# Optimization experiments

Hardware: AMD Instinct MI355X
Metric: run time of the kernel (lower is better)

## Reference

```python
import jax, jax.numpy as jnp
import numpy as np


def setup_inputs() -> dict:
    key = jax.random.key(0)
    k1, k2, k3, k4, k5 = jax.random.split(key, 5)
    B, C, H, W = 16, 256, 32, 32
    G = 4
    gd = C // G
    x = jax.random.normal(k1, (B, C, H, W), dtype=jnp.float32)
    # grouped 1x1 convs == per-group [gd, gd] linear maps (torch weight (C, C//G, 1, 1))
    s = 1.0 / np.sqrt(gd)
    wq = jax.random.normal(k2, (G, gd, gd), dtype=jnp.float32) * s
    wk = jax.random.normal(k3, (G, gd, gd), dtype=jnp.float32) * s
    wv = jax.random.normal(k4, (G, gd, gd), dtype=jnp.float32) * s
    wo = jax.random.normal(k5, (C, C), dtype=jnp.float32) * (1.0 / np.sqrt(C))
    return {"x": x, "wq": wq, "wk": wk, "wv": wv, "wo": wo}


def reference(x, wq, wk, wv, wo):
    B, C, H, W = x.shape
    G, gd = wq.shape[0], wq.shape[1]
    N = H * W
    xg = x.reshape(B, G, gd, N)  # split channels into groups, flatten spatial
    # grouped 1x1 conv projections: out[d] = sum_c w[d,c] * x[c] per group
    Q = jnp.einsum('bgcn,gdc->bgdn', xg, wq)
    K = jnp.einsum('bgcn,gdc->bgdn', xg, wk)
    V = jnp.einsum('bgcn,gdc->bgdn', xg, wv)
    scale = 1.0 / (float(gd) ** 0.5)
    # scores: Q^T K over channel dim -> [B, G, N, N]
    scores = jnp.einsum('bgdn,bgdm->bgnm', Q, K) * scale
    attn = jax.nn.softmax(scores, axis=-1)
    # out[d, n] = sum_m attn[n, m] * V[d, m]  (== (attn @ V^T)^T in torch code)
    out = jnp.einsum('bgnm,bgdm->bgdn', attn, V)
    out = out.reshape(B, C, H, W)
    # out_proj: dense 1x1 conv over all channels
    return jnp.einsum('bchw,dc->bdhw', out, wo)
```

## Files before the change

### kernel.cpp

```cpp
#include <hip/hip_runtime.h>
#include <hip/hip_bf16.h>


typedef __bf16 bf16x8 __attribute__((ext_vector_type(8)));
typedef short s16x8 __attribute__((ext_vector_type(8)));
typedef short s16x4 __attribute__((ext_vector_type(4)));
typedef float f32x4 __attribute__((ext_vector_type(4)));

__device__ __forceinline__ unsigned short f2b(float f) {
  unsigned int u = __builtin_bit_cast(unsigned int, f);
  u += 0x7fffu + ((u >> 16) & 1u);
  return (unsigned short)(u >> 16);
}
__device__ __forceinline__ unsigned short bf16u(float f) {
  return __builtin_bit_cast(unsigned short, __float2bfloat16(f));
}
__device__ __forceinline__ f32x4 mfma16(s16x8 a, s16x8 b, f32x4 c) {
  return __builtin_amdgcn_mfma_f32_16x16x32_bf16(
      __builtin_bit_cast(bf16x8, a), __builtin_bit_cast(bf16x8, b), c, 0, 0, 0);
}
__device__ __forceinline__ f32x4 mfma16k16(s16x4 a, s16x4 b, f32x4 c) {
  return __builtin_amdgcn_mfma_f32_16x16x16bf16_1k(a, b, c, 0, 0, 0);
}
__device__ __forceinline__ void gload16(const void* g, void* l) {
  __builtin_amdgcn_global_load_lds((const __attribute__((address_space(1))) void*)g,
                                   (__attribute__((address_space(3))) void*)l, 16, 0, 0);
}
__device__ __forceinline__ void stage8k(const unsigned short* g, short* l, int wid, int lane) {
  gload16(g + wid * 1024 + lane * 8,       l + wid * 1024);
  gload16(g + wid * 1024 + 512 + lane * 8, l + wid * 1024 + 512);
}

__global__ __launch_bounds__(256) void cvt_prep_kernel(
    const float* __restrict__ x, const float* __restrict__ wq, const float* __restrict__ wk,
    const float* __restrict__ wv, const float* __restrict__ wo,
    unsigned short* __restrict__ XbT, unsigned short* __restrict__ Xbs,
    unsigned short* __restrict__ Mts, unsigned short* __restrict__ Ub) {
  __shared__ __align__(16) short T[64][72];
  const int f = blockIdx.x;
  const int tid = threadIdx.x;
  if (f >= 1024) {
    int pb = f - 1024;
    if (pb < 64) {
      int id = pb * 256 + tid;
      int g = id >> 12, e = (id >> 6) & 63, c = id & 63;
      const float* q = wq + g * 4096;
      const float* k = wk + g * 4096;
      float acc = 0.f;
      for (int d = 0; d < 64; ++d) acc += q[d * 64 + c] * k[d * 64 + e];
      Mts[g * 4096 + e * 64 + (c ^ ((e & 7) << 3))] = f2b(acc * 0.125f * 1.4426950408889634f);
    } else {
      int i = (pb - 64) * 256 + tid;
      int o = i >> 8, gc = i & 255, g = gc >> 6, c = gc & 63;
      const float* v = wv + g * 4096;
      const float* w = wo + o * 256 + g * 64;
      float acc = 0.f;
      for (int d = 0; d < 64; ++d) acc += w[d] * v[d * 64 + c];
      Ub[i] = f2b(acc);
    }
    return;
  }
  const int xcd = f & 7;
  const int idx = f >> 3;
  const int head = ((idx & 7) << 3) | xcd;
  const int tile = idx >> 3;
  const int chunk = head * 16 + tile;
  const float* Xg = x + (size_t)head * 65536 + tile * 64;
  for (int i = 0; i < 4; ++i) {
    int row = i * 16 + (tid >> 4);
    int col = (tid & 15) * 4;
    float4 v = *(const float4*)(Xg + (size_t)row * 1024 + col);
    ushort4 s4 = make_ushort4(f2b(v.x), f2b(v.y), f2b(v.z), f2b(v.w));
    *(ushort4*)&T[row][col] = s4;
  }
  __syncthreads();
  unsigned short* oT = XbT + (size_t)chunk * 4096;
  unsigned short* oC = Xbs + (size_t)chunk * 4096;
  for (int p = 0; p < 2; ++p) {
    int idx2 = p * 256 + tid;
    int rr = idx2 >> 3, j = idx2 & 7;
    int sb = (j ^ (rr & 7)) * 8;
    unsigned short w[8];
    for (int i = 0; i < 8; ++i) w[i] = (unsigned short)T[sb + i][rr];
    *(s16x8*)(oT + rr * 64 + j * 8) = *(s16x8*)w;
    s16x8 rv = *(const s16x8*)&T[rr][sb];
    *(s16x8*)(oC + rr * 64 + j * 8) = rv;
  }
}

__global__ __launch_bounds__(256, 2)
void attn_kernel(const unsigned short* __restrict__ XbT, const unsigned short* __restrict__ Xbs,
                 const unsigned short* __restrict__ Mts, unsigned short* __restrict__ Ast) {
  __shared__ __align__(16) short XB[6][4096];

  const int f = blockIdx.x;
  const int bg = (f & 7) + ((f >> 6) << 3);
  const int n0 = ((f >> 3) & 7) * 128;
  const int tid = threadIdx.x;
  const int wid = tid >> 6;
  const int lane = tid & 63;
  const int l15 = lane & 15, l4 = lane >> 4;
  const int swz = (l15 & 7) << 3;
  const int l4h = l4 >> 1, l4l = (l4 & 1) * 4;
  const int nh = wid & 1;
  const int mh = wid >> 1;
  const unsigned short* xtg = XbT + (size_t)bg * 65536;
  const unsigned short* xcg = Xbs + (size_t)bg * 65536;

  stage8k(Mts + (bg & 3) * 4096, &XB[3][0], wid, lane);
  stage8k(xtg + (size_t)(n0 >> 6) * 4096, &XB[0][0], wid, lane);
  stage8k(xtg + (size_t)((n0 >> 6) + 1) * 4096, &XB[1][0], wid, lane);
  __syncthreads();

  s16x8 qpB[4][2];
  {
    s16x8 bm[4][2];
    for (int eb = 0; eb < 4; ++eb)
      for (int kc = 0; kc < 2; ++kc)
        bm[eb][kc] = *(const s16x8*)&XB[3][(eb * 16 + l15) * 64 + ((kc * 32 + l4 * 8) ^ swz)];
    for (int nt = 0; nt < 2; ++nt) {
      int q = wid * 32 + nt * 16;
      int h = q >> 6, rl = (q & 63) + l15;
      int rsw = ((rl & 7) << 3);
      s16x8 a0 = *(const s16x8*)&XB[h][rl * 64 + ((l4 * 8) ^ rsw)];
      s16x8 a1 = *(const s16x8*)&XB[h][rl * 64 + ((32 + l4 * 8) ^ rsw)];
      short* Qs = (q >= 64) ? &XB[5][0] : &XB[2][0];
      for (int eb = 0; eb < 4; ++eb) {
        f32x4 acc0 = {0.f, 0.f, 0.f, 0.f};
        acc0 = mfma16(a0, bm[eb][0], acc0);
        acc0 = mfma16(a1, bm[eb][1], acc0);
        for (int r = 0; r < 4; ++r) {
          int qrow = q + 4 * l4 + r;
          int cb2 = eb * 2 + (l15 >> 3);
          Qs[(qrow & 63) * 64 + (((cb2 ^ (qrow & 7)) << 3) | (l15 & 7))] = (short)bf16u(acc0[r]);
        }
      }
    }
  }
  asm volatile("s_waitcnt lgkmcnt(0)" ::: "memory");
  __builtin_amdgcn_sched_barrier(0);
  __syncthreads();
  {
    const short* Qs = nh ? &XB[5][0] : &XB[2][0];
#pragma unroll
    for (int nt = 0; nt < 4; ++nt) {
      int row = nt * 16 + l15;
#pragma unroll
      for (int kc = 0; kc < 2; ++kc)
        qpB[nt][kc] = *(const s16x8*)&Qs[row * 64 + (((kc * 4 + l4) ^ (l15 & 7)) << 3)];
    }
  }
  __syncthreads();

  stage8k(xtg,        &XB[0][0], wid, lane);
  stage8k(xcg,        &XB[3][0], wid, lane);
  stage8k(xtg + 4096, &XB[1][0], wid, lane);
  stage8k(xcg + 4096, &XB[4][0], wid, lane);

  float rowSp[4];
#pragma unroll
  for (int nt = 0; nt < 4; ++nt) rowSp[nt] = 0.f;
  f32x4 acc[4][4];
#pragma unroll
  for (int nt = 0; nt < 4; ++nt)
#pragma unroll
    for (int cb = 0; cb < 4; ++cb) acc[nt][cb] = (f32x4){0.f, 0.f, 0.f, 0.f};

#define STEP(K, VMC)                                                                    \
  {                                                                                     \
    asm volatile("s_waitcnt vmcnt(" VMC ")" ::: "memory");                              \
    __builtin_amdgcn_s_barrier();                                                       \
    __builtin_amdgcn_sched_barrier(0);                                                  \
    if ((K) < 14) {                                                                     \
      stage8k(xtg + (size_t)((K) + 2) * 4096, &XB[((K) + 2) % 3][0], wid, lane);        \
      stage8k(xcg + (size_t)((K) + 2) * 4096, &XB[3 + ((K) + 2) % 3][0], wid, lane);    \
    }                                                                                   \
    const int cs = (K) % 3;                                                             \
    _Pragma("unroll")                                                                   \
    for (int mb = 0; mb < 2; ++mb) {                                                    \
      const int rmr = (mh * 32 + mb * 16 + l15) * 64;                                   \
      s16x8 xt0 = *(const s16x8*)&XB[cs][rmr + ((l4 * 8) ^ swz)];                       \
      s16x8 xt1 = *(const s16x8*)&XB[cs][rmr + ((32 + l4 * 8) ^ swz)];                  \
      s16x4 ax4[4];                                                                     \
      _Pragma("unroll")                                                                 \
      for (int cb = 0; cb < 4; ++cb) {                                                  \
        int rc = cb * 16 + l15;                                                         \
        ax4[cb] = *(const s16x4*)&XB[3 + cs][rc * 64 +                                  \
                      (((mh * 4 + mb * 2 + l4h) ^ (rc & 7)) << 3) + l4l];               \
      }                                                                                 \
      _Pragma("unroll")                                                                 \
      for (int nt = 0; nt < 4; ++nt) {                                                  \
        f32x4 sv = {0.f, 0.f, 0.f, 0.f};                                                \
        sv = mfma16(xt0, qpB[nt][0], sv);                                               \
        sv = mfma16(xt1, qpB[nt][1], sv);                                               \
        float p0 = __builtin_amdgcn_exp2f(sv[0]);                                       \
        float p1 = __builtin_amdgcn_exp2f(sv[1]);                                       \
        float p2 = __builtin_amdgcn_exp2f(sv[2]);                                       \
        float p3 = __builtin_amdgcn_exp2f(sv[3]);                                       \
        rowSp[nt] += (p0 + p1) + (p2 + p3);                                             \
        unsigned int lo = (unsigned int)bf16u(p0) | ((unsigned int)bf16u(p1) << 16);    \
        unsigned int hi = (unsigned int)bf16u(p2) | ((unsigned int)bf16u(p3) << 16);    \
        uint2 pu; pu.x = lo; pu.y = hi;                                                 \
        s16x4 pb = __builtin_bit_cast(s16x4, pu);                                       \
        _Pragma("unroll")                                                               \
        for (int cb = 0; cb < 4; ++cb)                                                  \
          acc[nt][cb] = mfma16k16(ax4[cb], pb, acc[nt][cb]);                            \
      }                                                                                 \
    }                                                                                   \
  }

  STEP(0, "4")  STEP(1, "4")  STEP(2, "4")  STEP(3, "4")
  STEP(4, "4")  STEP(5, "4")  STEP(6, "4")  STEP(7, "4")
  STEP(8, "4")  STEP(9, "4")  STEP(10, "4") STEP(11, "4")
  STEP(12, "4") STEP(13, "4") STEP(14, "4") STEP(15, "0")
#undef STEP

  __syncthreads();
  float* Scr = (float*)&XB[0][0];

  float rs[4];
#pragma unroll
  for (int nt = 0; nt < 4; ++nt) {
    float t = rowSp[nt];
    t += __shfl_xor(t, 16, 64);
    t += __shfl_xor(t, 32, 64);
    rs[nt] = t;
  }

  if (mh == 1) {
#pragma unroll
    for (int nt = 0; nt < 4; ++nt) {
#pragma unroll
      for (int cb = 0; cb < 4; ++cb) {
        int base = ((nh * 4 + nt) * 4 + cb) * 256;
#pragma unroll
        for (int r = 0; r < 4; ++r)
          Scr[base + (l4 * 4 + r) * 16 + l15] = acc[nt][cb][r];
      }
      if (l4 == 0) Scr[8192 + (nh * 4 + nt) * 16 + l15] = rs[nt];
    }
  }
  __syncthreads();
  if (mh == 0) {
    const int b = bg >> 2, g = bg & 3;
#pragma unroll
    for (int nt = 0; nt < 4; ++nt) {
      float inv = 1.f / (rs[nt] + Scr[8192 + (nh * 4 + nt) * 16 + l15]);
      int n = n0 + nh * 64 + nt * 16 + l15;
      unsigned short* Ag = Ast + ((size_t)(b * 1024 + n)) * 256 + g * 64;
#pragma unroll
      for (int cb = 0; cb < 4; ++cb) {
        int base = ((nh * 4 + nt) * 4 + cb) * 256;
        float v0 = acc[nt][cb][0] + Scr[base + (l4 * 4 + 0) * 16 + l15];
        float v1 = acc[nt][cb][1] + Scr[base + (l4 * 4 + 1) * 16 + l15];
        float v2 = acc[nt][cb][2] + Scr[base + (l4 * 4 + 2) * 16 + l15];
        float v3 = acc[nt][cb][3] + Scr[base + (l4 * 4 + 3) * 16 + l15];
        ushort4 pk = make_ushort4(bf16u(v0 * inv), bf16u(v1 * inv),
                                  bf16u(v2 * inv), bf16u(v3 * inv));
        *(ushort4*)(Ag + cb * 16 + l4 * 4) = pk;
      }
    }
  }
}

__global__ __launch_bounds__(256, 2)
void proj_kernel(const unsigned short* __restrict__ Ub, const unsigned short* __restrict__ Ast,
                 float* __restrict__ out) {
  const int b = blockIdx.z;
  const int o0 = blockIdx.y * 128;
  const int n0 = blockIdx.x * 128;
  const int tid = threadIdx.x;
  const int wid = tid >> 6;
  const int lane = tid & 63;
  const int l15 = lane & 15, l4 = lane >> 4;
  const int ow = o0 + (wid & 1) * 64;
  const int nw = n0 + (wid >> 1) * 64;
  const unsigned short* A_ = Ast + ((size_t)b * 1024 + nw) * 256;

  f32x4 acc[4][4];
  for (int i = 0; i < 4; ++i)
    for (int j = 0; j < 4; ++j) acc[i][j] = (f32x4){0.f, 0.f, 0.f, 0.f};

  for (int kc = 0; kc < 8; ++kc) {
    s16x8 af[4], bfr[4];
    for (int ob = 0; ob < 4; ++ob)
      af[ob] = *(const s16x8*)(Ub + (size_t)(ow + ob * 16 + l15) * 256 + kc * 32 + l4 * 8);
    for (int nb = 0; nb < 4; ++nb)
      bfr[nb] = *(const s16x8*)(A_ + (size_t)(nb * 16 + l15) * 256 + kc * 32 + l4 * 8);
    for (int ob = 0; ob < 4; ++ob)
      for (int nb = 0; nb < 4; ++nb)
        acc[ob][nb] = mfma16(af[ob], bfr[nb], acc[ob][nb]);
  }
  float* O = out + ((size_t)b * 256 + ow) * 1024 + nw;
  for (int ob = 0; ob < 4; ++ob)
    for (int r = 0; r < 4; ++r)
      for (int nb = 0; nb < 4; ++nb)
        O[(size_t)(ob * 16 + l4 * 4 + r) * 1024 + nb * 16 + l15] = acc[ob][nb][r];
}

extern "C" void kernel_launch(void* const* d_in, const int* in_sizes, int n_in,
                              void* d_out, int out_size, void* d_ws, size_t ws_size,
                              hipStream_t stream) {
  const float* x  = (const float*)d_in[0];
  const float* wq = (const float*)d_in[1];
  const float* wk = (const float*)d_in[2];
  const float* wv = (const float*)d_in[3];
  const float* wo = (const float*)d_in[4];
  float* out = (float*)d_out;
  char* ws = (char*)d_ws;
  unsigned short* XbT = (unsigned short*)(ws);
  unsigned short* Xbs = (unsigned short*)(ws + 8388608);
  unsigned short* Mts = (unsigned short*)(ws + 16777216);
  unsigned short* Ub  = (unsigned short*)(ws + 16777216 + 32768);
  unsigned short* Ast = (unsigned short*)(ws + 16777216 + 163840);

  cvt_prep_kernel<<<1344, 256, 0, stream>>>(x, wq, wk, wv, wo, XbT, Xbs, Mts, Ub);
  attn_kernel<<<512, 256, 0, stream>>>(XbT, Xbs, Mts, Ast);
  proj_kernel<<<dim3(8, 2, 16), 256, 0, stream>>>(Ub, Ast, out);
}
```

Measured before the change: 51.68 us.

## Use per-wave private LDS slots with interleaved X layout, drop block barriers in attention loop

Prep now writes X into a combined per-half layout, so each key chunk's transposed and channel-major halves sit next to each other. Each wave in the attention kernel then streams only the half it needs into its own double-buffered LDS slots. This removes the block-wide barrier per step and lets waves run independently. The cost is wave-private loads that duplicate some traffic, plus an lgkmcnt wait before restaging. The projection kernel also halves its N tile per block to launch twice as many blocks.

```diff
diff --git a/kernel.cpp b/kernel.cpp
--- a/kernel.cpp
+++ b/kernel.cpp
@@ -34,8 +34,8 @@
 __global__ __launch_bounds__(256) void cvt_prep_kernel(
     const float* __restrict__ x, const float* __restrict__ wq, const float* __restrict__ wk,
     const float* __restrict__ wv, const float* __restrict__ wo,
-    unsigned short* __restrict__ XbT, unsigned short* __restrict__ Xbs,
-    unsigned short* __restrict__ Mts, unsigned short* __restrict__ Ub) {
+    unsigned short* __restrict__ XbH, unsigned short* __restrict__ Mts,
+    unsigned short* __restrict__ Ub) {
   __shared__ __align__(16) short T[64][72];
   const int f = blockIdx.x;
   const int tid = threadIdx.x;
@@ -64,34 +64,39 @@
   const int idx = f >> 3;
   const int head = ((idx & 7) << 3) | xcd;
   const int tile = idx >> 3;
-  const int chunk = head * 16 + tile;
   const float* Xg = x + (size_t)head * 65536 + tile * 64;
   for (int i = 0; i < 4; ++i) {
-    int row = i * 16 + (tid >> 4);
-    int col = (tid & 15) * 4;
-    float4 v = *(const float4*)(Xg + (size_t)row * 1024 + col);
+    int c = i * 16 + (tid >> 4);
+    int ml = (tid & 15) * 4;
+    float4 v = *(const float4*)(Xg + (size_t)c * 1024 + ml);
     ushort4 s4 = make_ushort4(f2b(v.x), f2b(v.y), f2b(v.z), f2b(v.w));
-    *(ushort4*)&T[row][col] = s4;
-  }
-  __syncthreads();
-  unsigned short* oT = XbT + (size_t)chunk * 4096;
-  unsigned short* oC = Xbs + (size_t)chunk * 4096;
-  for (int p = 0; p < 2; ++p) {
-    int idx2 = p * 256 + tid;
-    int rr = idx2 >> 3, j = idx2 & 7;
-    int sb = (j ^ (rr & 7)) * 8;
-    unsigned short w[8];
-    for (int i = 0; i < 8; ++i) w[i] = (unsigned short)T[sb + i][rr];
-    *(s16x8*)(oT + rr * 64 + j * 8) = *(s16x8*)w;
-    s16x8 rv = *(const s16x8*)&T[rr][sb];
-    *(s16x8*)(oC + rr * 64 + j * 8) = rv;
+    *(ushort4*)&T[c][ml] = s4;
+  }
+  __syncthreads();
+  unsigned short* out = XbH + ((size_t)head * 16 + tile) * 8192;
+  const int half = tid >> 7, rem = tid & 127;
+  {
+    int lr = rem >> 2, cp = (rem & 3) * 2;
+    for (int u = 0; u < 2; ++u) {
+      int cb8 = cp + u, pos = cb8 ^ (lr & 7);
+      unsigned short w[8];
+      for (int ci = 0; ci < 8; ++ci) w[ci] = (unsigned short)T[cb8 * 8 + ci][half * 32 + lr];
+      *(s16x8*)(out + half * 4096 + lr * 64 + pos * 8) = *(s16x8*)w;
+    }
+  }
+  {
+    int c = rem >> 1, j = (rem & 1) * 2;
+    s16x8 v0 = *(const s16x8*)&T[c][half * 32 + j * 8];
+    s16x8 v1 = *(const s16x8*)&T[c][half * 32 + j * 8 + 8];
+    *(s16x8*)(out + half * 4096 + 2048 + c * 32 + ((j ^ (c & 3)) * 8)) = v0;
+    *(s16x8*)(out + half * 4096 + 2048 + c * 32 + (((j + 1) ^ (c & 3)) * 8)) = v1;
   }
 }
 
 __global__ __launch_bounds__(256, 2)
-void attn_kernel(const unsigned short* __restrict__ XbT, const unsigned short* __restrict__ Xbs,
-                 const unsigned short* __restrict__ Mts, unsigned short* __restrict__ Ast) {
-  __shared__ __align__(16) short XB[6][4096];
+void attn_kernel(const unsigned short* __restrict__ XbH, const unsigned short* __restrict__ Mts,
+                 unsigned short* __restrict__ Ast) {
+  __shared__ __align__(16) short L[32768];
 
   const int f = blockIdx.x;
   const int bg = (f & 7) + ((f >> 6) << 3);
@@ -104,12 +109,14 @@
   const int l4h = l4 >> 1, l4l = (l4 & 1) * 4;
   const int nh = wid & 1;
   const int mh = wid >> 1;
-  const unsigned short* xtg = XbT + (size_t)bg * 65536;
-  const unsigned short* xcg = Xbs + (size_t)bg * 65536;
-
-  stage8k(Mts + (bg & 3) * 4096, &XB[3][0], wid, lane);
-  stage8k(xtg + (size_t)(n0 >> 6) * 4096, &XB[0][0], wid, lane);
-  stage8k(xtg + (size_t)((n0 >> 6) + 1) * 4096, &XB[1][0], wid, lane);
+  const unsigned short* xgh = XbH + (size_t)bg * 131072;
+
+  const int c0 = n0 >> 6;
+  stage8k(Mts + (bg & 3) * 4096, &L[0], wid, lane);
+  stage8k(xgh + (size_t)c0 * 8192,            &L[4096],  wid, lane);
+  stage8k(xgh + (size_t)c0 * 8192 + 4096,     &L[8192],  wid, lane);
+  stage8k(xgh + (size_t)(c0 + 1) * 8192,      &L[12288], wid, lane);
+  stage8k(xgh + (size_t)(c0 + 1) * 8192 + 4096, &L[16384], wid, lane);
   __syncthreads();
 
   s16x8 qpB[4][2];
@@ -117,22 +124,22 @@
     s16x8 bm[4][2];
     for (int eb = 0; eb < 4; ++eb)
       for (int kc = 0; kc < 2; ++kc)
-        bm[eb][kc] = *(const s16x8*)&XB[3][(eb * 16 + l15) * 64 + ((kc * 32 + l4 * 8) ^ swz)];
-    for (int nt = 0; nt < 2; ++nt) {
-      int q = wid * 32 + nt * 16;
-      int h = q >> 6, rl = (q & 63) + l15;
-      int rsw = ((rl & 7) << 3);
-      s16x8 a0 = *(const s16x8*)&XB[h][rl * 64 + ((l4 * 8) ^ rsw)];
-      s16x8 a1 = *(const s16x8*)&XB[h][rl * 64 + ((32 + l4 * 8) ^ rsw)];
-      short* Qs = (q >= 64) ? &XB[5][0] : &XB[2][0];
+        bm[eb][kc] = *(const s16x8*)&L[(eb * 16 + l15) * 64 + ((kc * 32 + l4 * 8) ^ swz)];
+    for (int nt2 = 0; nt2 < 2; ++nt2) {
+      int q0 = wid * 32 + nt2 * 16;
+      int base = 4096 + (q0 >> 6) * 8192 + ((q0 >> 5) & 1) * 4096;
+      int rl = (q0 & 31) + l15;
+      s16x8 a0 = *(const s16x8*)&L[base + rl * 64 + ((l4 * 8) ^ swz)];
+      s16x8 a1 = *(const s16x8*)&L[base + rl * 64 + ((32 + l4 * 8) ^ swz)];
+      short* Qs = &L[20480 + (q0 >= 64 ? 4096 : 0)];
       for (int eb = 0; eb < 4; ++eb) {
-        f32x4 acc0 = {0.f, 0.f, 0.f, 0.f};
-        acc0 = mfma16(a0, bm[eb][0], acc0);
-        acc0 = mfma16(a1, bm[eb][1], acc0);
+        f32x4 a = {0.f, 0.f, 0.f, 0.f};
+        a = mfma16(a0, bm[eb][0], a);
+        a = mfma16(a1, bm[eb][1], a);
         for (int r = 0; r < 4; ++r) {
-          int qrow = q + 4 * l4 + r;
+          int qrow = q0 + 4 * l4 + r;
           int cb2 = eb * 2 + (l15 >> 3);
-          Qs[(qrow & 63) * 64 + (((cb2 ^ (qrow & 7)) << 3) | (l15 & 7))] = (short)bf16u(acc0[r]);
+          Qs[(qrow & 63) * 64 + (((cb2 ^ (qrow & 7)) << 3) | (l15 & 7))] = (short)bf16u(a[r]);
         }
       }
     }
@@ -141,7 +148,7 @@
   __builtin_amdgcn_sched_barrier(0);
   __syncthreads();
   {
-    const short* Qs = nh ? &XB[5][0] : &XB[2][0];
+    const short* Qs = &L[20480 + (nh ? 4096 : 0)];
 #pragma unroll
     for (int nt = 0; nt < 4; ++nt) {
       int row = nt * 16 + l15;
@@ -152,10 +159,19 @@
   }
   __syncthreads();
 
-  stage8k(xtg,        &XB[0][0], wid, lane);
-  stage8k(xcg,        &XB[3][0], wid, lane);
-  stage8k(xtg + 4096, &XB[1][0], wid, lane);
-  stage8k(xcg + 4096, &XB[4][0], wid, lane);
+  const unsigned short* xgw = xgh + mh * 4096;
+  short* slot0 = &L[wid * 8192];
+  short* slot1 = &L[wid * 8192 + 4096];
+
+#define STAGEP(K, SL)                                                                   \
+  {                                                                                     \
+    const unsigned short* g_ = xgw + (size_t)(K) * 8192;                                \
+    _Pragma("unroll")                                                                   \
+    for (int i = 0; i < 8; ++i) gload16(g_ + i * 512 + lane * 8, (SL) + i * 512);       \
+  }
+
+  STAGEP(0, slot0)
+  STAGEP(1, slot1)
 
   float rowSp[4];
 #pragma unroll
@@ -169,24 +185,19 @@
 #define STEP(K, VMC)                                                                    \
   {                                                                                     \
     asm volatile("s_waitcnt vmcnt(" VMC ")" ::: "memory");                              \
-    __builtin_amdgcn_s_barrier();                                                       \
     __builtin_amdgcn_sched_barrier(0);                                                  \
-    if ((K) < 14) {                                                                     \
-      stage8k(xtg + (size_t)((K) + 2) * 4096, &XB[((K) + 2) % 3][0], wid, lane);        \
-      stage8k(xcg + (size_t)((K) + 2) * 4096, &XB[3 + ((K) + 2) % 3][0], wid, lane);    \
-    }                                                                                   \
-    const int cs = (K) % 3;                                                             \
+    short* cs = ((K) & 1) ? slot1 : slot0;                                              \
     _Pragma("unroll")                                                                   \
     for (int mb = 0; mb < 2; ++mb) {                                                    \
-      const int rmr = (mh * 32 + mb * 16 + l15) * 64;                                   \
-      s16x8 xt0 = *(const s16x8*)&XB[cs][rmr + ((l4 * 8) ^ swz)];                       \
-      s16x8 xt1 = *(const s16x8*)&XB[cs][rmr + ((32 + l4 * 8) ^ swz)];                  \
+      int rml = mb * 16 + l15;                                                          \
+      s16x8 xt0 = *(const s16x8*)&cs[rml * 64 + ((l4 * 8) ^ swz)];                      \
+      s16x8 xt1 = *(const s16x8*)&cs[rml * 64 + ((32 + l4 * 8) ^ swz)];                 \
       s16x4 ax4[4];                                                                     \
       _Pragma("unroll")                                                                 \
       for (int cb = 0; cb < 4; ++cb) {                                                  \
         int rc = cb * 16 + l15;                                                         \
-        ax4[cb] = *(const s16x4*)&XB[3 + cs][rc * 64 +                                  \
-                      (((mh * 4 + mb * 2 + l4h) ^ (rc & 7)) << 3) + l4l];               \
+        ax4[cb] = *(const s16x4*)&cs[2048 + rc * 32 +                                   \
+                        (((mb * 2 + l4h) ^ (rc & 3)) << 3) + l4l];                      \
       }                                                                                 \
       _Pragma("unroll")                                                                 \
       for (int nt = 0; nt < 4; ++nt) {                                                  \
@@ -207,16 +218,21 @@
           acc[nt][cb] = mfma16k16(ax4[cb], pb, acc[nt][cb]);                            \
       }                                                                                 \
     }                                                                                   \
-  }
-
-  STEP(0, "4")  STEP(1, "4")  STEP(2, "4")  STEP(3, "4")
-  STEP(4, "4")  STEP(5, "4")  STEP(6, "4")  STEP(7, "4")
-  STEP(8, "4")  STEP(9, "4")  STEP(10, "4") STEP(11, "4")
-  STEP(12, "4") STEP(13, "4") STEP(14, "4") STEP(15, "0")
+    if ((K) <= 13) {                                                                    \
+      asm volatile("s_waitcnt lgkmcnt(0)" ::: "memory");                                \
+      STAGEP((K) + 2, cs)                                                               \
+    }                                                                                   \
+  }
+
+  STEP(0, "8")  STEP(1, "8")  STEP(2, "8")  STEP(3, "8")
+  STEP(4, "8")  STEP(5, "8")  STEP(6, "8")  STEP(7, "8")
+  STEP(8, "8")  STEP(9, "8")  STEP(10, "8") STEP(11, "8")
+  STEP(12, "8") STEP(13, "8") STEP(14, "8") STEP(15, "0")
 #undef STEP
-
-  __syncthreads();
-  float* Scr = (float*)&XB[0][0];
+#undef STAGEP
+
+  __syncthreads();
+  float* Scr = (float*)&L[0];
 
   float rs[4];
 #pragma unroll
@@ -268,33 +284,33 @@
                  float* __restrict__ out) {
   const int b = blockIdx.z;
   const int o0 = blockIdx.y * 128;
-  const int n0 = blockIdx.x * 128;
+  const int n0 = blockIdx.x * 64;
   const int tid = threadIdx.x;
   const int wid = tid >> 6;
   const int lane = tid & 63;
   const int l15 = lane & 15, l4 = lane >> 4;
   const int ow = o0 + (wid & 1) * 64;
-  const int nw = n0 + (wid >> 1) * 64;
+  const int nw = n0 + (wid >> 1) * 32;
   const unsigned short* A_ = Ast + ((size_t)b * 1024 + nw) * 256;
 
-  f32x4 acc[4][4];
+  f32x4 acc[4][2];
   for (int i = 0; i < 4; ++i)
-    for (int j = 0; j < 4; ++j) acc[i][j] = (f32x4){0.f, 0.f, 0.f, 0.f};
+    for (int j = 0; j < 2; ++j) acc[i][j] = (f32x4){0.f, 0.f, 0.f, 0.f};
 
   for (int kc = 0; kc < 8; ++kc) {
-    s16x8 af[4], bfr[4];
+    s16x8 af[4], bfr[2];
     for (int ob = 0; ob < 4; ++ob)
       af[ob] = *(const s16x8*)(Ub + (size_t)(ow + ob * 16 + l15) * 256 + kc * 32 + l4 * 8);
-    for (int nb = 0; nb < 4; ++nb)
+    for (int nb = 0; nb < 2; ++nb)
       bfr[nb] = *(const s16x8*)(A_ + (size_t)(nb * 16 + l15) * 256 + kc * 32 + l4 * 8);
     for (int ob = 0; ob < 4; ++ob)
-      for (int nb = 0; nb < 4; ++nb)
+      for (int nb = 0; nb < 2; ++nb)
         acc[ob][nb] = mfma16(af[ob], bfr[nb], acc[ob][nb]);
   }
   float* O = out + ((size_t)b * 256 + ow) * 1024 + nw;
   for (int ob = 0; ob < 4; ++ob)
     for (int r = 0; r < 4; ++r)
-      for (int nb = 0; nb < 4; ++nb)
+      for (int nb = 0; nb < 2; ++nb)
         O[(size_t)(ob * 16 + l4 * 4 + r) * 1024 + nb * 16 + l15] = acc[ob][nb][r];
 }
 
@@ -308,13 +324,12 @@
   const float* wo = (const float*)d_in[4];
   float* out = (float*)d_out;
   char* ws = (char*)d_ws;
-  unsigned short* XbT = (unsigned short*)(ws);
-  unsigned short* Xbs = (unsigned short*)(ws + 8388608);
+  unsigned short* XbH = (unsigned short*)(ws);
   unsigned short* Mts = (unsigned short*)(ws + 16777216);
   unsigned short* Ub  = (unsigned short*)(ws + 16777216 + 32768);
   unsigned short* Ast = (unsigned short*)(ws + 16777216 + 163840);
 
-  cvt_prep_kernel<<<1344, 256, 0, stream>>>(x, wq, wk, wv, wo, XbT, Xbs, Mts, Ub);
-  attn_kernel<<<512, 256, 0, stream>>>(XbT, Xbs, Mts, Ast);
-  proj_kernel<<<dim3(8, 2, 16), 256, 0, stream>>>(Ub, Ast, out);
-}
+  cvt_prep_kernel<<<1344, 256, 0, stream>>>(x, wq, wk, wv, wo, XbH, Mts, Ub);
+  attn_kernel<<<512, 256, 0, stream>>>(XbH, Mts, Ast);
+  proj_kernel<<<dim3(16, 2, 16), 256, 0, stream>>>(Ub, Ast, out);
+}
```

New measurement: 58.00 us. +12.2%, slower.

## Halve attention query tile to 64, double-buffer LDS, and split key range across warps

Applied to the files above, without the earlier changes.

The attention kernel now processes 64 query rows per block instead of 128, doubling the grid to 1024 blocks. LDS shrinks from six to four 8K buffers with double buffering instead of triple, and launch bounds rise to 3 blocks per CU. All four warps share the queries and each takes a quarter of the keys, so the cross-warp reduction becomes a three-way sum done in two phases through LDS. The projection kernel's n-tile is also halved, doubling its grid. The aim is more occupancy and parallelism, at the cost of shallower prefetch, redundant K/V loading per block and extra reduction syncs.

```diff
diff --git a/kernel.cpp b/kernel.cpp
--- a/kernel.cpp
+++ b/kernel.cpp
@@ -88,60 +88,58 @@
   }
 }
 
-__global__ __launch_bounds__(256, 2)
+__global__ __launch_bounds__(256, 3)
 void attn_kernel(const unsigned short* __restrict__ XbT, const unsigned short* __restrict__ Xbs,
                  const unsigned short* __restrict__ Mts, unsigned short* __restrict__ Ast) {
-  __shared__ __align__(16) short XB[6][4096];
+  __shared__ __align__(16) short L[16384];
 
   const int f = blockIdx.x;
-  const int bg = (f & 7) + ((f >> 6) << 3);
-  const int n0 = ((f >> 3) & 7) * 128;
+  const int xcd = f & 7;
+  const int qt = (f >> 3) & 15;
+  const int bg = xcd + ((f >> 7) << 3);
+  const int n0 = qt * 64;
   const int tid = threadIdx.x;
   const int wid = tid >> 6;
   const int lane = tid & 63;
   const int l15 = lane & 15, l4 = lane >> 4;
   const int swz = (l15 & 7) << 3;
   const int l4h = l4 >> 1, l4l = (l4 & 1) * 4;
-  const int nh = wid & 1;
-  const int mh = wid >> 1;
+  const int rm = wid * 16 + l15;
   const unsigned short* xtg = XbT + (size_t)bg * 65536;
   const unsigned short* xcg = Xbs + (size_t)bg * 65536;
 
-  stage8k(Mts + (bg & 3) * 4096, &XB[3][0], wid, lane);
-  stage8k(xtg + (size_t)(n0 >> 6) * 4096, &XB[0][0], wid, lane);
-  stage8k(xtg + (size_t)((n0 >> 6) + 1) * 4096, &XB[1][0], wid, lane);
+  stage8k(Mts + (bg & 3) * 4096, &L[0], wid, lane);
+  stage8k(xtg + (size_t)qt * 4096, &L[4096], wid, lane);
   __syncthreads();
 
   s16x8 qpB[4][2];
   {
     s16x8 bm[4][2];
+#pragma unroll
     for (int eb = 0; eb < 4; ++eb)
+#pragma unroll
       for (int kc = 0; kc < 2; ++kc)
-        bm[eb][kc] = *(const s16x8*)&XB[3][(eb * 16 + l15) * 64 + ((kc * 32 + l4 * 8) ^ swz)];
-    for (int nt = 0; nt < 2; ++nt) {
-      int q = wid * 32 + nt * 16;
-      int h = q >> 6, rl = (q & 63) + l15;
-      int rsw = ((rl & 7) << 3);
-      s16x8 a0 = *(const s16x8*)&XB[h][rl * 64 + ((l4 * 8) ^ rsw)];
-      s16x8 a1 = *(const s16x8*)&XB[h][rl * 64 + ((32 + l4 * 8) ^ rsw)];
-      short* Qs = (q >= 64) ? &XB[5][0] : &XB[2][0];
-      for (int eb = 0; eb < 4; ++eb) {
-        f32x4 acc0 = {0.f, 0.f, 0.f, 0.f};
-        acc0 = mfma16(a0, bm[eb][0], acc0);
-        acc0 = mfma16(a1, bm[eb][1], acc0);
-        for (int r = 0; r < 4; ++r) {
-          int qrow = q + 4 * l4 + r;
-          int cb2 = eb * 2 + (l15 >> 3);
-          Qs[(qrow & 63) * 64 + (((cb2 ^ (qrow & 7)) << 3) | (l15 & 7))] = (short)bf16u(acc0[r]);
-        }
+        bm[eb][kc] = *(const s16x8*)&L[(eb * 16 + l15) * 64 + ((kc * 32 + l4 * 8) ^ swz)];
+    int rl = wid * 16 + l15;
+    s16x8 a0 = *(const s16x8*)&L[4096 + rl * 64 + ((l4 * 8) ^ swz)];
+    s16x8 a1 = *(const s16x8*)&L[4096 + rl * 64 + ((32 + l4 * 8) ^ swz)];
+    short* Qs = &L[8192];
+#pragma unroll
+    for (int eb = 0; eb < 4; ++eb) {
+      f32x4 a = {0.f, 0.f, 0.f, 0.f};
+      a = mfma16(a0, bm[eb][0], a);
+      a = mfma16(a1, bm[eb][1], a);
+#pragma unroll
+      for (int r = 0; r < 4; ++r) {
+        int qrow = wid * 16 + 4 * l4 + r;
+        int cb2 = eb * 2 + (l15 >> 3);
+        Qs[qrow * 64 + (((cb2 ^ (qrow & 7)) << 3) | (l15 & 7))] = (short)bf16u(a[r]);
       }
     }
   }
-  asm volatile("s_waitcnt lgkmcnt(0)" ::: "memory");
-  __builtin_amdgcn_sched_barrier(0);
   __syncthreads();
   {
-    const short* Qs = nh ? &XB[5][0] : &XB[2][0];
+    const short* Qs = &L[8192];
 #pragma unroll
     for (int nt = 0; nt < 4; ++nt) {
       int row = nt * 16 + l15;
@@ -152,10 +150,8 @@
   }
   __syncthreads();
 
-  stage8k(xtg,        &XB[0][0], wid, lane);
-  stage8k(xcg,        &XB[3][0], wid, lane);
-  stage8k(xtg + 4096, &XB[1][0], wid, lane);
-  stage8k(xcg + 4096, &XB[4][0], wid, lane);
+  stage8k(xtg, &L[0], wid, lane);
+  stage8k(xcg, &L[4096], wid, lane);
 
   float rowSp[4];
 #pragma unroll
@@ -166,57 +162,46 @@
 #pragma unroll
     for (int cb = 0; cb < 4; ++cb) acc[nt][cb] = (f32x4){0.f, 0.f, 0.f, 0.f};
 
-#define STEP(K, VMC)                                                                    \
-  {                                                                                     \
-    asm volatile("s_waitcnt vmcnt(" VMC ")" ::: "memory");                              \
-    __builtin_amdgcn_s_barrier();                                                       \
-    __builtin_amdgcn_sched_barrier(0);                                                  \
-    if ((K) < 14) {                                                                     \
-      stage8k(xtg + (size_t)((K) + 2) * 4096, &XB[((K) + 2) % 3][0], wid, lane);        \
-      stage8k(xcg + (size_t)((K) + 2) * 4096, &XB[3 + ((K) + 2) % 3][0], wid, lane);    \
-    }                                                                                   \
-    const int cs = (K) % 3;                                                             \
-    _Pragma("unroll")                                                                   \
-    for (int mb = 0; mb < 2; ++mb) {                                                    \
-      const int rmr = (mh * 32 + mb * 16 + l15) * 64;                                   \
-      s16x8 xt0 = *(const s16x8*)&XB[cs][rmr + ((l4 * 8) ^ swz)];                       \
-      s16x8 xt1 = *(const s16x8*)&XB[cs][rmr + ((32 + l4 * 8) ^ swz)];                  \
-      s16x4 ax4[4];                                                                     \
-      _Pragma("unroll")                                                                 \
-      for (int cb = 0; cb < 4; ++cb) {                                                  \
-        int rc = cb * 16 + l15;                                                         \
-        ax4[cb] = *(const s16x4*)&XB[3 + cs][rc * 64 +                                  \
-                      (((mh * 4 + mb * 2 + l4h) ^ (rc & 7)) << 3) + l4l];               \
-      }                                                                                 \
-      _Pragma("unroll")                                                                 \
-      for (int nt = 0; nt < 4; ++nt) {                                                  \
-        f32x4 sv = {0.f, 0.f, 0.f, 0.f};                                                \
-        sv = mfma16(xt0, qpB[nt][0], sv);                                               \
-        sv = mfma16(xt1, qpB[nt][1], sv);                                               \
-        float p0 = __builtin_amdgcn_exp2f(sv[0]);                                       \
-        float p1 = __builtin_amdgcn_exp2f(sv[1]);                                       \
-        float p2 = __builtin_amdgcn_exp2f(sv[2]);                                       \
-        float p3 = __builtin_amdgcn_exp2f(sv[3]);                                       \
-        rowSp[nt] += (p0 + p1) + (p2 + p3);                                             \
-        unsigned int lo = (unsigned int)bf16u(p0) | ((unsigned int)bf16u(p1) << 16);    \
-        unsigned int hi = (unsigned int)bf16u(p2) | ((unsigned int)bf16u(p3) << 16);    \
-        uint2 pu; pu.x = lo; pu.y = hi;                                                 \
-        s16x4 pb = __builtin_bit_cast(s16x4, pu);                                       \
-        _Pragma("unroll")                                                               \
-        for (int cb = 0; cb < 4; ++cb)                                                  \
-          acc[nt][cb] = mfma16k16(ax4[cb], pb, acc[nt][cb]);                            \
-      }                                                                                 \
-    }                                                                                   \
-  }
-
-  STEP(0, "4")  STEP(1, "4")  STEP(2, "4")  STEP(3, "4")
-  STEP(4, "4")  STEP(5, "4")  STEP(6, "4")  STEP(7, "4")
-  STEP(8, "4")  STEP(9, "4")  STEP(10, "4") STEP(11, "4")
-  STEP(12, "4") STEP(13, "4") STEP(14, "4") STEP(15, "0")
-#undef STEP
-
-  __syncthreads();
-  float* Scr = (float*)&XB[0][0];
+#pragma unroll
+  for (int K = 0; K < 16; ++K) {
+    __syncthreads();
+    if (K < 15) {
+      const int dst = ((K + 1) & 1) * 8192;
+      stage8k(xtg + (size_t)(K + 1) * 4096, &L[dst], wid, lane);
+      stage8k(xcg + (size_t)(K + 1) * 4096, &L[dst + 4096], wid, lane);
+    }
+    const int so = (K & 1) * 8192;
+    s16x8 xt0 = *(const s16x8*)&L[so + rm * 64 + ((l4 * 8) ^ swz)];
+    s16x8 xt1 = *(const s16x8*)&L[so + rm * 64 + ((32 + l4 * 8) ^ swz)];
+    s16x4 ax4[4];
+#pragma unroll
+    for (int cb = 0; cb < 4; ++cb) {
+      int rc = cb * 16 + l15;
+      ax4[cb] = *(const s16x4*)&L[so + 4096 + rc * 64 +
+                                  (((wid * 2 + l4h) ^ (rc & 7)) << 3) + l4l];
+    }
+#pragma unroll
+    for (int nt = 0; nt < 4; ++nt) {
+      f32x4 sv = {0.f, 0.f, 0.f, 0.f};
+      sv = mfma16(xt0, qpB[nt][0], sv);
+      sv = mfma16(xt1, qpB[nt][1], sv);
+      float p0 = __builtin_amdgcn_exp2f(sv[0]);
+      float p1 = __builtin_amdgcn_exp2f(sv[1]);
+      float p2 = __builtin_amdgcn_exp2f(sv[2]);
+      float p3 = __builtin_amdgcn_exp2f(sv[3]);
+      rowSp[nt] += (p0 + p1) + (p2 + p3);
+      unsigned int lo = (unsigned int)bf16u(p0) | ((unsigned int)bf16u(p1) << 16);
+      unsigned int hi = (unsigned int)bf16u(p2) | ((unsigned int)bf16u(p3) << 16);
+      uint2 pu; pu.x = lo; pu.y = hi;
+      s16x4 pb = __builtin_bit_cast(s16x4, pu);
+#pragma unroll
+      for (int cb = 0; cb < 4; ++cb)
+        acc[nt][cb] = mfma16k16(ax4[cb], pb, acc[nt][cb]);
+    }
+  }
+
+  __syncthreads();
+  float* Scr = (float*)&L[0];
 
   float rs[4];
 #pragma unroll
@@ -227,36 +212,78 @@
     rs[nt] = t;
   }
 
-  if (mh == 1) {
-#pragma unroll
-    for (int nt = 0; nt < 4; ++nt) {
+  if (wid != 0) {
+#pragma unroll
+    for (int nt = 0; nt < 4; ++nt)
+      if (l4 == 0) Scr[6144 + (wid - 1) * 64 + nt * 16 + l15] = rs[nt];
+#pragma unroll
+    for (int h = 0; h < 2; ++h)
+#pragma unroll
+      for (int cb = 0; cb < 4; ++cb)
+#pragma unroll
+        for (int r = 0; r < 4; ++r)
+          Scr[((wid - 1) * 2 + h) * 1024 + (cb * 16 + l4 * 4 + r) * 16 + l15] = acc[h][cb][r];
+  }
+  __syncthreads();
+  const int b = bg >> 2, g = bg & 3;
+  float inv[4];
+  if (wid == 0) {
+#pragma unroll
+    for (int nt = 0; nt < 4; ++nt)
+      inv[nt] = 1.f / (rs[nt] + Scr[6144 + nt * 16 + l15] +
+                       Scr[6208 + nt * 16 + l15] + Scr[6272 + nt * 16 + l15]);
+#pragma unroll
+    for (int h = 0; h < 2; ++h) {
+      int n = n0 + h * 16 + l15;
+      unsigned short* Ag = Ast + ((size_t)(b * 1024 + n)) * 256 + g * 64;
 #pragma unroll
       for (int cb = 0; cb < 4; ++cb) {
-        int base = ((nh * 4 + nt) * 4 + cb) * 256;
+        float v0 = acc[h][cb][0], v1 = acc[h][cb][1];
+        float v2 = acc[h][cb][2], v3 = acc[h][cb][3];
+#pragma unroll
+        for (int w = 1; w < 4; ++w) {
+          int base = ((w - 1) * 2 + h) * 1024 + (cb * 16 + l4 * 4) * 16 + l15;
+          v0 += Scr[base];
+          v1 += Scr[base + 16];
+          v2 += Scr[base + 32];
+          v3 += Scr[base + 48];
+        }
+        ushort4 pk = make_ushort4(bf16u(v0 * inv[h]), bf16u(v1 * inv[h]),
+                                  bf16u(v2 * inv[h]), bf16u(v3 * inv[h]));
+        *(ushort4*)(Ag + cb * 16 + l4 * 4) = pk;
+      }
+    }
+  }
+  __syncthreads();
+  if (wid != 0) {
+#pragma unroll
+    for (int h = 0; h < 2; ++h)
+#pragma unroll
+      for (int cb = 0; cb < 4; ++cb)
 #pragma unroll
         for (int r = 0; r < 4; ++r)
-          Scr[base + (l4 * 4 + r) * 16 + l15] = acc[nt][cb][r];
-      }
-      if (l4 == 0) Scr[8192 + (nh * 4 + nt) * 16 + l15] = rs[nt];
-    }
-  }
-  __syncthreads();
-  if (mh == 0) {
-    const int b = bg >> 2, g = bg & 3;
-#pragma unroll
-    for (int nt = 0; nt < 4; ++nt) {
-      float inv = 1.f / (rs[nt] + Scr[8192 + (nh * 4 + nt) * 16 + l15]);
-      int n = n0 + nh * 64 + nt * 16 + l15;
+          Scr[((wid - 1) * 2 + h) * 1024 + (cb * 16 + l4 * 4 + r) * 16 + l15] = acc[2 + h][cb][r];
+  }
+  __syncthreads();
+  if (wid == 0) {
+#pragma unroll
+    for (int h = 0; h < 2; ++h) {
+      int n = n0 + (2 + h) * 16 + l15;
       unsigned short* Ag = Ast + ((size_t)(b * 1024 + n)) * 256 + g * 64;
 #pragma unroll
       for (int cb = 0; cb < 4; ++cb) {
-        int base = ((nh * 4 + nt) * 4 + cb) * 256;
-        float v0 = acc[nt][cb][0] + Scr[base + (l4 * 4 + 0) * 16 + l15];
-        float v1 = acc[nt][cb][1] + Scr[base + (l4 * 4 + 1) * 16 + l15];
-        float v2 = acc[nt][cb][2] + Scr[base + (l4 * 4 + 2) * 16 + l15];
-        float v3 = acc[nt][cb][3] + Scr[base + (l4 * 4 + 3) * 16 + l15];
-        ushort4 pk = make_ushort4(bf16u(v0 * inv), bf16u(v1 * inv),
-                                  bf16u(v2 * inv), bf16u(v3 * inv));
+        float v0 = acc[2 + h][cb][0], v1 = acc[2 + h][cb][1];
+        float v2 = acc[2 + h][cb][2], v3 = acc[2 + h][cb][3];
+#pragma unroll
+        for (int w = 1; w < 4; ++w) {
+          int base = ((w - 1) * 2 + h) * 1024 + (cb * 16 + l4 * 4) * 16 + l15;
+          v0 += Scr[base];
+          v1 += Scr[base + 16];
+          v2 += Scr[base + 32];
+          v3 += Scr[base + 48];
+        }
+        ushort4 pk = make_ushort4(bf16u(v0 * inv[2 + h]), bf16u(v1 * inv[2 + h]),
+                                  bf16u(v2 * inv[2 + h]), bf16u(v3 * inv[2 + h]));
         *(ushort4*)(Ag + cb * 16 + l4 * 4) = pk;
       }
     }
@@ -268,33 +295,33 @@
                  float* __restrict__ out) {
   const int b = blockIdx.z;
   const int o0 = blockIdx.y * 128;
-  const int n0 = blockIdx.x * 128;
+  const int n0 = blockIdx.x * 64;
   const int tid = threadIdx.x;
   const int wid = tid >> 6;
   const int lane = tid & 63;
   const int l15 = lane & 15, l4 = lane >> 4;
   const int ow = o0 + (wid & 1) * 64;
-  const int nw = n0 + (wid >> 1) * 64;
+  const int nw = n0 + (wid >> 1) * 32;
   const unsigned short* A_ = Ast + ((size_t)b * 1024 + nw) * 256;
 
-  f32x4 acc[4][4];
+  f32x4 acc[4][2];
   for (int i = 0; i < 4; ++i)
-    for (int j = 0; j < 4; ++j) acc[i][j] = (f32x4){0.f, 0.f, 0.f, 0.f};
+    for (int j = 0; j < 2; ++j) acc[i][j] = (f32x4){0.f, 0.f, 0.f, 0.f};
 
   for (int kc = 0; kc < 8; ++kc) {
-    s16x8 af[4], bfr[4];
+    s16x8 af[4], bfr[2];
     for (int ob = 0; ob < 4; ++ob)
       af[ob] = *(const s16x8*)(Ub + (size_t)(ow + ob * 16 + l15) * 256 + kc * 32 + l4 * 8);
-    for (int nb = 0; nb < 4; ++nb)
+    for (int nb = 0; nb < 2; ++nb)
       bfr[nb] = *(const s16x8*)(A_ + (size_t)(nb * 16 + l15) * 256 + kc * 32 + l4 * 8);
     for (int ob = 0; ob < 4; ++ob)
-      for (int nb = 0; nb < 4; ++nb)
+      for (int nb = 0; nb < 2; ++nb)
         acc[ob][nb] = mfma16(af[ob], bfr[nb], acc[ob][nb]);
   }
   float* O = out + ((size_t)b * 256 + ow) * 1024 + nw;
   for (int ob = 0; ob < 4; ++ob)
     for (int r = 0; r < 4; ++r)
-      for (int nb = 0; nb < 4; ++nb)
+      for (int nb = 0; nb < 2; ++nb)
         O[(size_t)(ob * 16 + l4 * 4 + r) * 1024 + nb * 16 + l15] = acc[ob][nb][r];
 }
 
@@ -315,6 +342,6 @@
   unsigned short* Ast = (unsigned short*)(ws + 16777216 + 163840);
 
   cvt_prep_kernel<<<1344, 256, 0, stream>>>(x, wq, wk, wv, wo, XbT, Xbs, Mts, Ub);
-  attn_kernel<<<512, 256, 0, stream>>>(XbT, Xbs, Mts, Ast);
-  proj_kernel<<<dim3(8, 2, 16), 256, 0, stream>>>(Ub, Ast, out);
-}
+  attn_kernel<<<1024, 256, 0, stream>>>(XbT, Xbs, Mts, Ast);
+  proj_kernel<<<dim3(16, 2, 16), 256, 0, stream>>>(Ub, Ast, out);
+}
```

New measurement: 101.2 us. 1.96x slower.
